# Kernel tuning notes

Measured on AMD Instinct MI355X. Metric: run time of the kernel, lower is better.

Reference implementation:

```python
import jax, jax.numpy as jnp
import numpy as np

N_FR, N_FV, N_REL, N_VAL, N_KN = 512, 512, 256, 256, 512
TOPK_FR, TOPK_FV, TOPK_REL, TOPK_VAL = 8, 8, 4, 6
EPS = 1e-8


def setup_inputs() -> dict:
    key = jax.random.key(0)
    k1, k2, k3, k4 = jax.random.split(key, 4)
    B, S, D, DS = 8, 2048, 2048, 64
    N = N_FR + N_FV + N_REL + N_VAL + N_KN  # 2304
    return {
        "x": jax.random.normal(k1, (B, S, D), dtype=jnp.float32),
        "importance": jax.random.uniform(k2, (B, S), dtype=jnp.float32),
        "W": jax.random.normal(k3, (DS, D), dtype=jnp.float32) * (1.0 / np.sqrt(D)),
        "b": jnp.zeros((DS,), dtype=jnp.float32),
        "neuron_emb": jax.random.normal(k4, (N, DS), dtype=jnp.float32) * 0.02,
    }


def _topk_sparsify(w, k):
    # w: [B, n] -> keep top-k values, zero the rest, renormalize to sum 1
    vals, idx = jax.lax.top_k(w, k)
    B = w.shape[0]
    sparse = jnp.zeros_like(w).at[jnp.arange(B)[:, None], idx].set(vals)
    return sparse / (sparse.sum(axis=-1, keepdims=True) + EPS)


def reference(x, importance, W, b, neuron_emb):
    # Projection (nn.Linear): [B,S,d_space]; dropout is identity in eval mode
    h = jnp.einsum('bsd,kd->bsk', x, W) + b
    # Normalized neuron embeddings (F.normalize along dim=-1)
    emb = neuron_emb / jnp.linalg.norm(neuron_emb, axis=-1, keepdims=True)
    # All routing logits in one shot: [B, S, total_neurons]
    all_logits = jnp.einsum('bsk,nk->bsn', h, emb)

    fr_end = N_FR
    fv_end = N_FR + N_FV
    rel_end = fv_end + N_REL
    val_end = rel_end + N_VAL

    fr_pref = jax.nn.softmax(all_logits[..., :fr_end], axis=-1)
    fv_pref = jax.nn.softmax(all_logits[..., fr_end:fv_end], axis=-1)
    rel_pref = jax.nn.softmax(all_logits[..., fv_end:rel_end], axis=-1)  # shared by Q and K
    val_pref = jax.nn.softmax(all_logits[..., rel_end:val_end], axis=-1)

    def dense(pref):
        return jnp.einsum('bs,bsn->bn', importance, pref)

    fr_w = _topk_sparsify(dense(fr_pref), TOPK_FR)
    fv_w = _topk_sparsify(dense(fv_pref), TOPK_FV)
    rel_d = dense(rel_pref)
    rq_w = _topk_sparsify(rel_d, TOPK_REL)
    rk_w = rq_w  # relational_Q and relational_K slices are identical
    val_w = _topk_sparsify(dense(val_pref), TOPK_VAL)

    # Concatenate the five per-batch routing weight vectors: [B, 512+512+256+256+256]
    return jnp.concatenate([fr_w, fv_w, rq_w, rk_w, val_w], axis=-1)
```

## Files before the change

### kernel.cpp

```cpp
#include <hip/hip_runtime.h>
#include <hip/hip_bf16.h>

#define B_    8
#define S_    2048
#define D_    2048
#define DS_   64
#define NUSED 1536
#define TOK   16384

typedef __attribute__((ext_vector_type(8))) short bf16x8;
typedef __attribute__((ext_vector_type(4))) float f32x4;

static constexpr int WS_ETF  = 0;
static constexpr int WS_HT   = 98304;
static constexpr int WS_PART = 2195456;
static constexpr int WS_PART2= 3768320;
static constexpr int WS_WF   = 3866624;

typedef __attribute__((address_space(1))) const void g_void;
typedef __attribute__((address_space(3))) void l_void;

__device__ inline short bf_hi(float f, float& rhi) {
    __hip_bfloat16 h = __float2bfloat16(f);
    rhi = __bfloat162float(h);
    return __builtin_bit_cast(short, h);
}
__device__ inline short bf_of(float f) {
    __hip_bfloat16 h = __float2bfloat16(f);
    return __builtin_bit_cast(short, h);
}
__device__ inline int sliceOfTile(int tile) {
    return tile < 32 ? 0 : tile < 64 ? 1 : tile < 80 ? 2 : 3;
}

__launch_bounds__(256)
__global__ void k_pre(const float* __restrict__ emb, const float* __restrict__ W,
                      short* __restrict__ etfrag, short* __restrict__ wfrag) {
    __shared__ float red[2][16][8];
    __shared__ float rn[2][16];
    const int tid = threadIdx.x;
    if (blockIdx.x < 48) {
        const int tl = tid >> 7, tid2 = tid & 127;
        const int kh = tid2 >> 6, lane = tid2 & 63;
        const int tile = blockIdx.x * 2 + tl;
        const int nl = lane & 15;
        const int n = tile * 16 + nl;
        const int kb = kh * 32 + (lane >> 4) * 8;
        const float* ep = emb + n * DS_ + kb;
        float4 a = *reinterpret_cast<const float4*>(ep);
        float4 b = *reinterpret_cast<const float4*>(ep + 4);
        float f[8] = {a.x, a.y, a.z, a.w, b.x, b.y, b.z, b.w};
        float ss = 0.f;
#pragma unroll
        for (int j = 0; j < 8; ++j) ss += f[j] * f[j];
        red[tl][nl][kh * 4 + (lane >> 4)] = ss;
        __syncthreads();
        if (tid2 < 16) {
            float s = 0.f;
#pragma unroll
            for (int j = 0; j < 8; ++j) s += red[tl][tid2][j];
            rn[tl][tid2] = 1.0f / sqrtf(s);
        }
        __syncthreads();
        const float r0 = rn[tl][nl];
        bf16x8 hi, lo;
#pragma unroll
        for (int j = 0; j < 8; ++j) {
            float v = f[j] * r0, r;
            hi[j] = bf_hi(v, r);
            lo[j] = bf_of(v - r);
        }
        short* dst = etfrag + (size_t)((tile * 2 + kh) * 64 + lane) * 16;
        *reinterpret_cast<bf16x8*>(dst)     = hi;
        *reinterpret_cast<bf16x8*>(dst + 8) = lo;
    } else {
        const int kstep = blockIdx.x - 48;
        const int msub = tid >> 6, lane = tid & 63;
        const int m = msub * 16 + (lane & 15);
        const float* wp = W + m * D_ + kstep * 32 + (lane >> 4) * 8;
        float4 a = *reinterpret_cast<const float4*>(wp);
        float4 b = *reinterpret_cast<const float4*>(wp + 4);
        float f[8] = {a.x, a.y, a.z, a.w, b.x, b.y, b.z, b.w};
        bf16x8 hi, lo;
#pragma unroll
        for (int j = 0; j < 8; ++j) {
            float r;
            hi[j] = bf_hi(f[j], r);
            lo[j] = bf_of(f[j] - r);
        }
        short* base = wfrag + (size_t)(kstep * 4 + msub) * 1024;
        *reinterpret_cast<bf16x8*>(base + lane * 8)       = hi;
        *reinterpret_cast<bf16x8*>(base + 512 + lane * 8) = lo;
    }
}

#define MFMA16(A, Bv, C) __builtin_amdgcn_mfma_f32_16x16x32_bf16(A, Bv, C, 0, 0, 0)

__launch_bounds__(256, 2)
__global__ void k_gemm1(const float* __restrict__ x, const short* __restrict__ wfrag,
                        float* __restrict__ htp) {
    __shared__ short wlds[2][2][4096];

    const int tid   = threadIdx.x;
    const int split = blockIdx.x & 1;
    const int tb    = (blockIdx.x >> 1) * 64;
    const int wave  = tid >> 6, lane = tid & 63;
    const int tok   = tb + wave * 16 + (lane & 15);

    const float* xp   = x + (size_t)tok * D_ + split * 1024 + (lane >> 4) * 8;
    const short* wsrc = wfrag + (size_t)(split * 32) * 4096;

    f32x4 acc0 = {0.f, 0.f, 0.f, 0.f};
    f32x4 acc1 = acc0, acc2 = acc0, acc3 = acc0;

#define STAGE(g, buf)                                                                        \
    {                                                                                        \
        const short* s0 = wsrc + (size_t)(2 * (g)) * 4096;                                   \
        __builtin_amdgcn_global_load_lds((g_void*)(s0 + tid * 8),                            \
                                         (l_void*)(&wlds[buf][0][tid * 8]), 16, 0, 0);       \
        __builtin_amdgcn_global_load_lds((g_void*)(s0 + 2048 + tid * 8),                     \
                                         (l_void*)(&wlds[buf][0][2048 + tid * 8]), 16, 0, 0);\
        __builtin_amdgcn_global_load_lds((g_void*)(s0 + 4096 + tid * 8),                     \
                                         (l_void*)(&wlds[buf][1][tid * 8]), 16, 0, 0);       \
        __builtin_amdgcn_global_load_lds((g_void*)(s0 + 6144 + tid * 8),                     \
                                         (l_void*)(&wlds[buf][1][2048 + tid * 8]), 16, 0, 0);\
    }

    STAGE(0, 0);
    float4 xc0 = *reinterpret_cast<const float4*>(xp);
    float4 xc1 = *reinterpret_cast<const float4*>(xp + 4);
    float4 xc2 = *reinterpret_cast<const float4*>(xp + 32);
    float4 xc3 = *reinterpret_cast<const float4*>(xp + 36);

#pragma unroll 2
    for (int g = 0; g < 16; ++g) {
        __syncthreads();
        const int buf = g & 1;
        float4 xn0, xn1, xn2, xn3;
        if (g < 15) {
            STAGE(g + 1, buf ^ 1);
            const float* nxp = xp + (size_t)(g + 1) * 64;
            xn0 = *reinterpret_cast<const float4*>(nxp);
            xn1 = *reinterpret_cast<const float4*>(nxp + 4);
            xn2 = *reinterpret_cast<const float4*>(nxp + 32);
            xn3 = *reinterpret_cast<const float4*>(nxp + 36);
        }
#pragma unroll
        for (int kk = 0; kk < 2; ++kk) {
            const float4 va = kk ? xc2 : xc0;
            const float4 vb = kk ? xc3 : xc1;
            float xf[8] = {va.x, va.y, va.z, va.w, vb.x, vb.y, vb.z, vb.w};
            bf16x8 bh, bl;
#pragma unroll
            for (int j = 0; j < 8; ++j) {
                float r;
                bh[j] = bf_hi(xf[j], r);
                bl[j] = bf_of(xf[j] - r);
            }
            const short* wl = &wlds[buf][kk][0];
            bf16x8 ah0 = *reinterpret_cast<const bf16x8*>(wl +    0 + lane * 8);
            bf16x8 al0 = *reinterpret_cast<const bf16x8*>(wl +  512 + lane * 8);
            bf16x8 ah1 = *reinterpret_cast<const bf16x8*>(wl + 1024 + lane * 8);
            bf16x8 al1 = *reinterpret_cast<const bf16x8*>(wl + 1536 + lane * 8);
            bf16x8 ah2 = *reinterpret_cast<const bf16x8*>(wl + 2048 + lane * 8);
            bf16x8 al2 = *reinterpret_cast<const bf16x8*>(wl + 2560 + lane * 8);
            bf16x8 ah3 = *reinterpret_cast<const bf16x8*>(wl + 3072 + lane * 8);
            bf16x8 al3 = *reinterpret_cast<const bf16x8*>(wl + 3584 + lane * 8);

            acc0 = MFMA16(ah0, bh, acc0);
            acc1 = MFMA16(ah1, bh, acc1);
            acc2 = MFMA16(ah2, bh, acc2);
            acc3 = MFMA16(ah3, bh, acc3);
            acc0 = MFMA16(al0, bh, acc0);
            acc1 = MFMA16(al1, bh, acc1);
            acc2 = MFMA16(al2, bh, acc2);
            acc3 = MFMA16(al3, bh, acc3);
            acc0 = MFMA16(ah0, bl, acc0);
            acc1 = MFMA16(ah1, bl, acc1);
            acc2 = MFMA16(ah2, bl, acc2);
            acc3 = MFMA16(ah3, bl, acc3);
        }
        if (g < 15) { xc0 = xn0; xc1 = xn1; xc2 = xn2; xc3 = xn3; }
    }

    const int row0 = split * 64 + (lane >> 4) * 4;
    const int col  = tb + wave * 16 + (lane & 15);
#pragma unroll
    for (int r = 0; r < 4; ++r) {
        htp[(size_t)(row0 +  0 + r) * TOK + col] = acc0[r];
        htp[(size_t)(row0 + 16 + r) * TOK + col] = acc1[r];
        htp[(size_t)(row0 + 32 + r) * TOK + col] = acc2[r];
        htp[(size_t)(row0 + 48 + r) * TOK + col] = acc3[r];
    }
}

__launch_bounds__(512, 4)
__global__ void k_route2(const float* __restrict__ htp, const float* __restrict__ bias,
                         const short* __restrict__ etfrag, const float* __restrict__ imp,
                         float* __restrict__ part) {
    __shared__ float h_lds[64][16];
    __shared__ float zw[8][2][16];
    __shared__ float coef[4][16];
    __shared__ float impb[16];

    const int tid = threadIdx.x;
    const int w = tid >> 6, lane = tid & 63;
    const int tt = blockIdx.x;
    const int tk = lane & 15, g = lane >> 4;

    if (tid < 256) {
        const int k = tid >> 2, t4 = (tid & 3) << 2;
        const float4* hp4 = reinterpret_cast<const float4*>(htp);
        const int col = tt * 4 + (tid & 3);
        float4 a = hp4[(size_t)k * 4096 + col];
        float4 b = hp4[(size_t)(k + 64) * 4096 + col];
        float bk = bias[k];
        float4 s;
        s.x = a.x + b.x + bk;
        s.y = a.y + b.y + bk;
        s.z = a.z + b.z + bk;
        s.w = a.w + b.w + bk;
        *reinterpret_cast<float4*>(&h_lds[k][t4]) = s;
    }
    if (tid < 16) impb[tid] = imp[tt * 16 + tid];
    __syncthreads();

    bf16x8 bh0, bl0, bh1, bl1;
#pragma unroll
    for (int j = 0; j < 8; ++j) {
        float r;
        float v0 = h_lds[g * 8 + j][tk];
        bh0[j] = bf_hi(v0, r);
        bl0[j] = bf_of(v0 - r);
        float v1 = h_lds[32 + g * 8 + j][tk];
        bh1[j] = bf_hi(v1, r);
        bl1[j] = bf_of(v1 - r);
    }

    const int t0 = w * 12;
    const int sA = sliceOfTile(t0);
    const int sB = sliceOfTile(t0 + 11);
    float zacc0 = 0.f, zacc1 = 0.f;
    float p[12][4];

    const short* ep = etfrag + (size_t)t0 * 2048 + lane * 16;
#pragma unroll
    for (int ti = 0; ti < 12; ++ti) {
        const short* cp = ep + (size_t)ti * 2048;
        bf16x8 ah0 = *reinterpret_cast<const bf16x8*>(cp);
        bf16x8 al0 = *reinterpret_cast<const bf16x8*>(cp + 8);
        bf16x8 ah1 = *reinterpret_cast<const bf16x8*>(cp + 1024);
        bf16x8 al1 = *reinterpret_cast<const bf16x8*>(cp + 1032);
        f32x4 a0 = {0.f, 0.f, 0.f, 0.f};
        f32x4 a1 = {0.f, 0.f, 0.f, 0.f};
        a0 = MFMA16(ah0, bh0, a0);
        a1 = MFMA16(ah1, bh1, a1);
        a0 = MFMA16(al0, bh0, a0);
        a1 = MFMA16(al1, bh1, a1);
        a0 = MFMA16(ah0, bl0, a0);
        a1 = MFMA16(ah1, bl1, a1);
        const float p0 = __expf(a0[0] + a1[0]);
        const float p1 = __expf(a0[1] + a1[1]);
        const float p2 = __expf(a0[2] + a1[2]);
        const float p3 = __expf(a0[3] + a1[3]);
        p[ti][0] = p0; p[ti][1] = p1; p[ti][2] = p2; p[ti][3] = p3;
        const float zs = (p0 + p1) + (p2 + p3);
        if (sliceOfTile(t0 + ti) == sA) zacc0 += zs; else zacc1 += zs;
    }

    zacc0 += __shfl_xor(zacc0, 16); zacc0 += __shfl_xor(zacc0, 32);
    zacc1 += __shfl_xor(zacc1, 16); zacc1 += __shfl_xor(zacc1, 32);
    if (lane < 16) { zw[w][0][lane] = zacc0; zw[w][1][lane] = zacc1; }
    __syncthreads();

    if (tid < 64) {
        const int s = tid >> 4, k2 = tid & 15;
        float z = 0.f;
#pragma unroll
        for (int w2 = 0; w2 < 8; ++w2) {
            const int a = sliceOfTile(w2 * 12);
            const int b = sliceOfTile(w2 * 12 + 11);
            if (a == s) z += zw[w2][0][k2];
            if (b == s && b != a) z += zw[w2][1][k2];
        }
        coef[s][k2] = impb[k2] / z;
    }
    __syncthreads();

    const float cA = coef[sA][tk];
    const float cB = coef[sB][tk];
    float* pout = part + (size_t)tt * NUSED;
#pragma unroll
    for (int ti = 0; ti < 12; ++ti) {
        const float c = (sliceOfTile(t0 + ti) == sA) ? cA : cB;
        float v0 = p[ti][0] * c, v1 = p[ti][1] * c, v2 = p[ti][2] * c, v3 = p[ti][3] * c;
#pragma unroll
        for (int st = 1; st < 16; st <<= 1) {
            v0 += __shfl_xor(v0, st);
            v1 += __shfl_xor(v1, st);
            v2 += __shfl_xor(v2, st);
            v3 += __shfl_xor(v3, st);
        }
        if (tk == 0)
            *reinterpret_cast<float4*>(&pout[(t0 + ti) * 16 + g * 4]) =
                make_float4(v0, v1, v2, v3);
    }
}

__launch_bounds__(256)
__global__ void kA(const float* __restrict__ part, float* __restrict__ part2) {
    const int tid = threadIdx.x;
    const int b = blockIdx.x >> 3, g = blockIdx.x & 7;
    const int base = (b * 128 + g * 16) * NUSED;
#pragma unroll
    for (int i = 0; i < 6; ++i) {
        int n = tid + 256 * i;
        float s = 0.f;
#pragma unroll
        for (int r = 0; r < 16; ++r) s += part[base + r * NUSED + n];
        part2[(b * 8 + g) * NUSED + n] = s;
    }
}

__launch_bounds__(256)
__global__ void kB(const float* __restrict__ part2, float* __restrict__ out) {
    __shared__ float dens[NUSED];
    __shared__ float s_v[4][8];
    __shared__ int   s_n[4][8];
    const int tid = threadIdx.x;
    const int b = blockIdx.x;

#pragma unroll
    for (int i = 0; i < 6; ++i) {
        int n = tid + 256 * i;
        float s = 0.f;
#pragma unroll
        for (int g = 0; g < 8; ++g) s += part2[(b * 8 + g) * NUSED + n];
        dens[n] = s;
    }
    for (int i = tid; i < 1792; i += 256) out[b * 1792 + i] = 0.f;
    __syncthreads();

    const int w = tid >> 6, lane = tid & 63;
    const int soffs[4] = {0, 512, 1024, 1280};
    const int ssz[4]   = {512, 512, 256, 256};
    const int kks[4]   = {8, 8, 4, 6};
    const int ooffs[4] = {0, 512, 1024, 1536};
    const int Sn = ssz[w], soff = soffs[w], kk = kks[w];
    const int nslots = Sn >> 6;

    float v[8];
#pragma unroll
    for (int i = 0; i < 8; ++i)
        v[i] = (i < nslots) ? dens[soff + lane + 64 * i] : -1e30f;

    unsigned rm = 0;
    float ssum = 0.f;
    for (int it = 0; it < kk; ++it) {
        float bv = -1e30f;
        int bn = 0x7fffffff;
#pragma unroll
        for (int i = 0; i < 8; ++i) {
            bool valid = (i < nslots) && !((rm >> i) & 1u);
            if (valid && v[i] > bv) { bv = v[i]; bn = lane + 64 * i; }
        }
#pragma unroll
        for (int off = 32; off; off >>= 1) {
            float ov = __shfl_xor(bv, off);
            int   on = __shfl_xor(bn, off);
            if (ov > bv || (ov == bv && on < bn)) { bv = ov; bn = on; }
        }
        ssum += bv;
        if ((bn & 63) == lane) rm |= 1u << (bn >> 6);
        if (lane == 0) { s_v[w][it] = bv; s_n[w][it] = bn; }
    }
    const float inv = 1.f / (ssum + 1e-8f);
    if (lane < kk) {
        int n = s_n[w][lane];
        float val = s_v[w][lane] * inv;
        out[b * 1792 + ooffs[w] + n] = val;
        if (w == 2) out[b * 1792 + 1280 + n] = val;
    }
}

extern "C" void kernel_launch(void* const* d_in, const int* in_sizes, int n_in,
                              void* d_out, int out_size, void* d_ws, size_t ws_size,
                              hipStream_t stream) {
    const float* x    = (const float*)d_in[0];
    const float* imp  = (const float*)d_in[1];
    const float* W    = (const float*)d_in[2];
    const float* bias = (const float*)d_in[3];
    const float* emb  = (const float*)d_in[4];
    float* out = (float*)d_out;
    float* ws  = (float*)d_ws;

    short* etfrag = (short*)(ws + WS_ETF);
    float* htp    = ws + WS_HT;
    float* part   = ws + WS_PART;
    float* part2  = ws + WS_PART2;
    short* wfrag  = (short*)(ws + WS_WF);

    k_pre<<<112, 256, 0, stream>>>(emb, W, etfrag, wfrag);
    k_gemm1<<<512, 256, 0, stream>>>(x, wfrag, htp);
    k_route2<<<1024, 512, 0, stream>>>(htp, bias, etfrag, imp, part);
    kA<<<64, 256, 0, stream>>>(part, part2);
    kB<<<8, 256, 0, stream>>>(part2, out);
}
```

Baseline: 79.86 us.

## Process 64 tokens per routing block and recompute logits instead of storing

The routing kernel now handles four 16-token tiles per block, so each embedding fragment loaded from global memory is reused across four token tiles, and the grid shrinks from 1024 to 256 blocks. Instead of keeping the 12x4 exponentials in registers between the normalizer pass and the output pass, it recomputes the MFMA logits and exp in a second pass. This cuts embedding-fragment traffic per token at the cost of doubled MFMA/exp work, fewer blocks (possibly under-filling the GPU's CUs) and a relaxed occupancy hint.

```diff
diff --git a/kernel.cpp b/kernel.cpp
--- a/kernel.cpp
+++ b/kernel.cpp
@@ -194,56 +194,62 @@
     }
 }
 
-__launch_bounds__(512, 4)
+__launch_bounds__(512)
 __global__ void k_route2(const float* __restrict__ htp, const float* __restrict__ bias,
                          const short* __restrict__ etfrag, const float* __restrict__ imp,
                          float* __restrict__ part) {
-    __shared__ float h_lds[64][16];
-    __shared__ float zw[8][2][16];
-    __shared__ float coef[4][16];
-    __shared__ float impb[16];
+    __shared__ float h_lds[64][64];
+    __shared__ float zw[8][2][4][16];
+    __shared__ float coef[4][64];
+    __shared__ float impb[64];
 
     const int tid = threadIdx.x;
     const int w = tid >> 6, lane = tid & 63;
-    const int tt = blockIdx.x;
+    const int tt64 = blockIdx.x;
     const int tk = lane & 15, g = lane >> 4;
 
-    if (tid < 256) {
-        const int k = tid >> 2, t4 = (tid & 3) << 2;
+    {
         const float4* hp4 = reinterpret_cast<const float4*>(htp);
-        const int col = tt * 4 + (tid & 3);
-        float4 a = hp4[(size_t)k * 4096 + col];
-        float4 b = hp4[(size_t)(k + 64) * 4096 + col];
-        float bk = bias[k];
-        float4 s;
-        s.x = a.x + b.x + bk;
-        s.y = a.y + b.y + bk;
-        s.z = a.z + b.z + bk;
-        s.w = a.w + b.w + bk;
-        *reinterpret_cast<float4*>(&h_lds[k][t4]) = s;
-    }
-    if (tid < 16) impb[tid] = imp[tt * 16 + tid];
+#pragma unroll
+        for (int i = 0; i < 2; ++i) {
+            const int idx = tid * 2 + i;
+            const int k = idx >> 4, c4 = idx & 15;
+            float4 a = hp4[(size_t)k * 4096 + tt64 * 16 + c4];
+            float4 b = hp4[(size_t)(k + 64) * 4096 + tt64 * 16 + c4];
+            float bk = bias[k];
+            float4 s;
+            s.x = a.x + b.x + bk;
+            s.y = a.y + b.y + bk;
+            s.z = a.z + b.z + bk;
+            s.w = a.w + b.w + bk;
+            *reinterpret_cast<float4*>(&h_lds[k][c4 * 4]) = s;
+        }
+    }
+    if (tid < 64) impb[tid] = imp[tt64 * 64 + tid];
     __syncthreads();
 
-    bf16x8 bh0, bl0, bh1, bl1;
-#pragma unroll
-    for (int j = 0; j < 8; ++j) {
-        float r;
-        float v0 = h_lds[g * 8 + j][tk];
-        bh0[j] = bf_hi(v0, r);
-        bl0[j] = bf_of(v0 - r);
-        float v1 = h_lds[32 + g * 8 + j][tk];
-        bh1[j] = bf_hi(v1, r);
-        bl1[j] = bf_of(v1 - r);
+    bf16x8 bh0[4], bl0[4], bh1[4], bl1[4];
+#pragma unroll
+    for (int tt = 0; tt < 4; ++tt) {
+#pragma unroll
+        for (int j = 0; j < 8; ++j) {
+            float r;
+            float v0 = h_lds[g * 8 + j][tt * 16 + tk];
+            bh0[tt][j] = bf_hi(v0, r);
+            bl0[tt][j] = bf_of(v0 - r);
+            float v1 = h_lds[32 + g * 8 + j][tt * 16 + tk];
+            bh1[tt][j] = bf_hi(v1, r);
+            bl1[tt][j] = bf_of(v1 - r);
+        }
     }
 
     const int t0 = w * 12;
     const int sA = sliceOfTile(t0);
     const int sB = sliceOfTile(t0 + 11);
-    float zacc0 = 0.f, zacc1 = 0.f;
-    float p[12][4];
-
     const short* ep = etfrag + (size_t)t0 * 2048 + lane * 16;
+
+    float z0[4] = {0.f, 0.f, 0.f, 0.f};
+    float z1[4] = {0.f, 0.f, 0.f, 0.f};
 #pragma unroll
     for (int ti = 0; ti < 12; ++ti) {
         const short* cp = ep + (size_t)ti * 2048;
@@ -251,59 +257,97 @@
         bf16x8 al0 = *reinterpret_cast<const bf16x8*>(cp + 8);
         bf16x8 ah1 = *reinterpret_cast<const bf16x8*>(cp + 1024);
         bf16x8 al1 = *reinterpret_cast<const bf16x8*>(cp + 1032);
-        f32x4 a0 = {0.f, 0.f, 0.f, 0.f};
-        f32x4 a1 = {0.f, 0.f, 0.f, 0.f};
-        a0 = MFMA16(ah0, bh0, a0);
-        a1 = MFMA16(ah1, bh1, a1);
-        a0 = MFMA16(al0, bh0, a0);
-        a1 = MFMA16(al1, bh1, a1);
-        a0 = MFMA16(ah0, bl0, a0);
-        a1 = MFMA16(ah1, bl1, a1);
-        const float p0 = __expf(a0[0] + a1[0]);
-        const float p1 = __expf(a0[1] + a1[1]);
-        const float p2 = __expf(a0[2] + a1[2]);
-        const float p3 = __expf(a0[3] + a1[3]);
-        p[ti][0] = p0; p[ti][1] = p1; p[ti][2] = p2; p[ti][3] = p3;
-        const float zs = (p0 + p1) + (p2 + p3);
-        if (sliceOfTile(t0 + ti) == sA) zacc0 += zs; else zacc1 += zs;
-    }
-
-    zacc0 += __shfl_xor(zacc0, 16); zacc0 += __shfl_xor(zacc0, 32);
-    zacc1 += __shfl_xor(zacc1, 16); zacc1 += __shfl_xor(zacc1, 32);
-    if (lane < 16) { zw[w][0][lane] = zacc0; zw[w][1][lane] = zacc1; }
+        const bool inA = (sliceOfTile(t0 + ti) == sA);
+#pragma unroll
+        for (int tt = 0; tt < 4; ++tt) {
+            f32x4 a0 = {0.f, 0.f, 0.f, 0.f};
+            f32x4 a1 = {0.f, 0.f, 0.f, 0.f};
+            a0 = MFMA16(ah0, bh0[tt], a0);
+            a1 = MFMA16(ah1, bh1[tt], a1);
+            a0 = MFMA16(al0, bh0[tt], a0);
+            a1 = MFMA16(al1, bh1[tt], a1);
+            a0 = MFMA16(ah0, bl0[tt], a0);
+            a1 = MFMA16(ah1, bl1[tt], a1);
+            const float p0 = __expf(a0[0] + a1[0]);
+            const float p1 = __expf(a0[1] + a1[1]);
+            const float p2 = __expf(a0[2] + a1[2]);
+            const float p3 = __expf(a0[3] + a1[3]);
+            const float zs = (p0 + p1) + (p2 + p3);
+            if (inA) z0[tt] += zs; else z1[tt] += zs;
+        }
+    }
+
+#pragma unroll
+    for (int tt = 0; tt < 4; ++tt) {
+        z0[tt] += __shfl_xor(z0[tt], 16); z0[tt] += __shfl_xor(z0[tt], 32);
+        z1[tt] += __shfl_xor(z1[tt], 16); z1[tt] += __shfl_xor(z1[tt], 32);
+    }
+    if (lane < 16) {
+#pragma unroll
+        for (int tt = 0; tt < 4; ++tt) {
+            zw[w][0][tt][lane] = z0[tt];
+            zw[w][1][tt][lane] = z1[tt];
+        }
+    }
     __syncthreads();
 
-    if (tid < 64) {
-        const int s = tid >> 4, k2 = tid & 15;
+    if (tid < 256) {
+        const int s = tid >> 6, tok = tid & 63;
+        const int tt = tok >> 4, k2 = tok & 15;
         float z = 0.f;
 #pragma unroll
         for (int w2 = 0; w2 < 8; ++w2) {
             const int a = sliceOfTile(w2 * 12);
             const int b = sliceOfTile(w2 * 12 + 11);
-            if (a == s) z += zw[w2][0][k2];
-            if (b == s && b != a) z += zw[w2][1][k2];
-        }
-        coef[s][k2] = impb[k2] / z;
+            if (a == s) z += zw[w2][0][tt][k2];
+            if (b == s && b != a) z += zw[w2][1][tt][k2];
+        }
+        coef[s][tok] = impb[tok] / z;
     }
     __syncthreads();
 
-    const float cA = coef[sA][tk];
-    const float cB = coef[sB][tk];
-    float* pout = part + (size_t)tt * NUSED;
+    float cA[4], cB[4];
+#pragma unroll
+    for (int tt = 0; tt < 4; ++tt) {
+        cA[tt] = coef[sA][tt * 16 + tk];
+        cB[tt] = coef[sB][tt * 16 + tk];
+    }
 #pragma unroll
     for (int ti = 0; ti < 12; ++ti) {
-        const float c = (sliceOfTile(t0 + ti) == sA) ? cA : cB;
-        float v0 = p[ti][0] * c, v1 = p[ti][1] * c, v2 = p[ti][2] * c, v3 = p[ti][3] * c;
-#pragma unroll
-        for (int st = 1; st < 16; st <<= 1) {
-            v0 += __shfl_xor(v0, st);
-            v1 += __shfl_xor(v1, st);
-            v2 += __shfl_xor(v2, st);
-            v3 += __shfl_xor(v3, st);
-        }
-        if (tk == 0)
-            *reinterpret_cast<float4*>(&pout[(t0 + ti) * 16 + g * 4]) =
-                make_float4(v0, v1, v2, v3);
+        const short* cp = ep + (size_t)ti * 2048;
+        bf16x8 ah0 = *reinterpret_cast<const bf16x8*>(cp);
+        bf16x8 al0 = *reinterpret_cast<const bf16x8*>(cp + 8);
+        bf16x8 ah1 = *reinterpret_cast<const bf16x8*>(cp + 1024);
+        bf16x8 al1 = *reinterpret_cast<const bf16x8*>(cp + 1032);
+        const int at = t0 + ti;
+        const bool inA = (sliceOfTile(at) == sA);
+#pragma unroll
+        for (int tt = 0; tt < 4; ++tt) {
+            f32x4 a0 = {0.f, 0.f, 0.f, 0.f};
+            f32x4 a1 = {0.f, 0.f, 0.f, 0.f};
+            a0 = MFMA16(ah0, bh0[tt], a0);
+            a1 = MFMA16(ah1, bh1[tt], a1);
+            a0 = MFMA16(al0, bh0[tt], a0);
+            a1 = MFMA16(al1, bh1[tt], a1);
+            a0 = MFMA16(ah0, bl0[tt], a0);
+            a1 = MFMA16(ah1, bl1[tt], a1);
+            const float c = inA ? cA[tt] : cB[tt];
+            float v0 = __expf(a0[0] + a1[0]) * c;
+            float v1 = __expf(a0[1] + a1[1]) * c;
+            float v2 = __expf(a0[2] + a1[2]) * c;
+            float v3 = __expf(a0[3] + a1[3]) * c;
+#pragma unroll
+            for (int st = 1; st < 16; st <<= 1) {
+                v0 += __shfl_xor(v0, st);
+                v1 += __shfl_xor(v1, st);
+                v2 += __shfl_xor(v2, st);
+                v3 += __shfl_xor(v3, st);
+            }
+            if (tk == 0)
+                *reinterpret_cast<float4*>(
+                    &part[(size_t)(tt64 * 4 + tt) * NUSED + at * 16 + g * 4]) =
+                    make_float4(v0, v1, v2, v3);
+        }
     }
 }
 
@@ -402,7 +446,7 @@
 
     k_pre<<<112, 256, 0, stream>>>(emb, W, etfrag, wfrag);
     k_gemm1<<<512, 256, 0, stream>>>(x, wfrag, htp);
-    k_route2<<<1024, 512, 0, stream>>>(htp, bias, etfrag, imp, part);
+    k_route2<<<256, 512, 0, stream>>>(htp, bias, etfrag, imp, part);
     kA<<<64, 256, 0, stream>>>(part, part2);
     kB<<<8, 256, 0, stream>>>(part2, out);
 }
```

New measurement: 81.80 us. 1.02x slower.
